# Performance work log

Measured on AMD Instinct MI355X. Metric: run time of the kernel, lower is better.

The kernel has to match this reference:

```python
import jax, jax.numpy as jnp
import numpy as np

H, HD, CHUNK = 16, 64, 128


def _rotary(x):
    # x: (B,H,N,d); rotary_embedding_torch default: interleaved pairs, theta=10000
    N, d = x.shape[-2], x.shape[-1]
    inv_freq = 1.0 / (10000.0 ** (jnp.arange(0, d, 2, dtype=jnp.float32) / d))
    ang = jnp.arange(N, dtype=jnp.float32)[:, None] * inv_freq[None, :]  # (N, d/2)
    ang = jnp.repeat(ang, 2, axis=-1)  # (N, d), each freq repeated twice
    cos, sin = jnp.cos(ang), jnp.sin(ang)
    x1, x2 = x[..., 0::2], x[..., 1::2]
    xr = jnp.stack([-x2, x1], axis=-1).reshape(x.shape)  # rotate_half (interleaved)
    return x * cos + xr * sin


def _split_heads(t, B, N):
    return t.reshape(B, N, H, HD).transpose(0, 2, 1, 3)  # (B,H,N,Hd)


def _chunked(Q, KK, VK):
    # chunk-parallel linear-attention recurrence: per-token outer products,
    # intra-chunk cumsum, carried state across chunks, Frobenius normalization.
    B, h, N, d = Q.shape
    nc = N // CHUNK

    def to_chunks(t):
        return t.reshape(B, h, nc, CHUNK, d).transpose(2, 0, 1, 3, 4)  # (nc,B,h,c,d)

    S0 = jnp.eye(d, dtype=Q.dtype) * jnp.sqrt(jnp.float32(d))
    S0 = jnp.broadcast_to(S0, (B, h, d, d))

    def step(SK_state, inp):
        q, kk, vk = inp  # (B,h,c,d)
        ok = jnp.einsum('bhni,bhnj->bhnij', kk, vk)            # outer products
        SK = jnp.cumsum(ok, axis=2) + SK_state[:, :, None]      # prefix-sum + carry
        norm = jnp.sqrt(jnp.sum(SK * SK, axis=(-2, -1), keepdims=True)) + 1e-8
        SKn = SK / norm                                         # Frobenius-normalized
        y = jnp.einsum('bhni,bhnji->bhnj', q, SKn)              # q @ SK^T per token
        return SK[:, :, -1], y

    _, ys = jax.lax.scan(step, S0, (to_chunks(Q), to_chunks(KK), to_chunks(VK)))
    return ys.transpose(1, 2, 0, 3, 4).reshape(B, h, N, d)


def setup_inputs():
    key = jax.random.key(0)
    ks = jax.random.split(key, 5)
    B, N, D = 2, 2048, 1024
    X = jax.random.normal(ks[0], (B, N, D), jnp.float32)
    w_qkv = jax.random.normal(ks[1], (D, 3 * H * HD), jnp.float32) * 0.02
    w_kvkv = jax.random.normal(ks[2], (D, 4 * H * HD), jnp.float32) * 0.02
    w_out = jax.random.normal(ks[3], (H * HD, D), jnp.float32) * 0.02
    b_out = jnp.zeros((D,), jnp.float32)
    return {"X": X, "w_qkv": w_qkv, "w_kvkv": w_kvkv, "w_out": w_out, "b_out": b_out}


def reference(X, w_qkv, w_kvkv, w_out, b_out):
    B, N, D = X.shape
    q, k, v = jnp.split(X @ w_qkv, 3, axis=-1)
    Q = _split_heads(q, B, N)
    K = _split_heads(k, B, N)
    V = _split_heads(v, B, N)
    kk, vk, _kv, _vv = jnp.split(X @ w_kvkv, 4, axis=-1)
    KK = _split_heads(kk, B, N)
    VK = _split_heads(vk, B, N)
    # NOTE: the SV branch (KV, VV) in the original is returned by the chunked fn
    # but never used by forward's output, so it is dead code for the fwd result.
    Qn = _chunked(Q, KK, VK)
    Qr = _rotary(Qn)
    Kr = _rotary(K)
    scale = 1.0 / jnp.sqrt(jnp.float32(HD))
    scores = jnp.einsum('bhqd,bhkd->bhqk', Qr, Kr) * scale
    mask = jnp.tril(jnp.ones((N, N), dtype=bool))
    scores = jnp.where(mask, scores, -jnp.inf)
    attn = jax.nn.softmax(scores, axis=-1)
    out = jnp.einsum('bhqk,bhkd->bhqd', attn, V)
    out = out.transpose(0, 2, 1, 3).reshape(B, N, H * HD)
    return out @ w_out + b_out
```

## Files before the change

kernel.cpp:

```cpp
#include <hip/hip_runtime.h>

typedef unsigned int u32;
typedef unsigned short u16;
typedef __attribute__((ext_vector_type(8))) __bf16 bf16x8;
typedef __attribute__((ext_vector_type(4))) float f32x4;

constexpr int NH = 16;
constexpr int HDM = 64;
constexpr int NSQ = 2048;
constexpr int KD = 1024;
constexpr int BHT = 32;
constexpr float ROT_C = 13.287712379549449f / 32.0f;

__device__ __forceinline__ u16 f2bf(float f) {
  u32 u = __float_as_uint(f);
  u += 0x7fffu + ((u >> 16) & 1u);
  return (u16)(u >> 16);
}
__device__ __forceinline__ float bf2f(u16 h) {
  return __uint_as_float(((u32)h) << 16);
}

__device__ __forceinline__ void fast_sincos(float th, float* s, float* c) {
  __sincosf(th, s, c);
}

__device__ __forceinline__ void gl_lds16(const u16* g, u16* l) {
  __builtin_amdgcn_global_load_lds(
      (const __attribute__((address_space(1))) u32*)g,
      (__attribute__((address_space(3))) u32*)l, 16, 0, 0);
}

__device__ __forceinline__ bf16x8 ldf(const u16* b, int row, int cb, int rs) {
  return *(const bf16x8*)((const char*)b + row * rs + ((cb * 16) ^ ((row & 7) << 4)));
}

__global__ void k_f32_to_bf16(const float* __restrict__ src, u16* __restrict__ dst, int n4) {
  int i = blockIdx.x * 256 + threadIdx.x;
  if (i < n4) {
    float4 v = ((const float4*)src)[i];
    ushort4 o;
    o.x = f2bf(v.x); o.y = f2bf(v.y); o.z = f2bf(v.z); o.w = f2bf(v.w);
    ((ushort4*)dst)[i] = o;
  }
}

__global__ void k_transpose_bf16(const float* __restrict__ src, int srcld,
                                 u16* __restrict__ dst, int dstld) {
  __shared__ float tile[64][65];
  int ct = blockIdx.x * 64, kt = blockIdx.y * 64;
  int lc = threadIdx.x & 63, rg = threadIdx.x >> 6;
#pragma unroll
  for (int i = 0; i < 16; ++i) {
    int kl = rg * 16 + i;
    tile[kl][lc] = src[(size_t)(kt + kl) * srcld + ct + lc];
  }
  __syncthreads();
#pragma unroll
  for (int i = 0; i < 16; ++i) {
    int cl = rg * 16 + i;
    dst[(size_t)(ct + cl) * dstld + kt + lc] = f2bf(tile[lc][cl]);
  }
}

template <int MODE>
__device__ __forceinline__ void gemm_stage(const u16* __restrict__ A, const u16* __restrict__ Bt,
                                           u16* Albuf, u16* Blbuf, int mt, int nt, int kt,
                                           int w, int lane) {
#pragma unroll
  for (int i = 0; i < 2; ++i) {
    int ob = (w * 2 + i) * 1024 + lane * 16;
    int row = ob >> 6;
    int ke = (ob & 63) >> 1;
    const u16* ga;
    if (MODE == 0) {
      ga = A + (size_t)(mt * 128 + row) * KD + kt * 32 + ke;
    } else {
      int grow = mt * 128 + row;
      int k = kt * 32 + ke;
      ga = A + ((size_t)((grow >> 11) * NH + (k >> 6)) * NSQ + (grow & 2047)) * HDM + (k & 63);
    }
    gl_lds16(ga, Albuf + (w * 2 + i) * 512);
    const u16* gb = Bt + (size_t)(nt * 128 + row) * KD + kt * 32 + ke;
    gl_lds16(gb, Blbuf + (w * 2 + i) * 512);
  }
}

__device__ __forceinline__ void gemm_compute(const u16* Albuf, const u16* Blbuf,
                                             f32x4 acc[4][4], int wr, int wc, int g, int q) {
  bf16x8 af[4], bfr[4];
#pragma unroll
  for (int m = 0; m < 4; ++m)
    af[m] = *(const bf16x8*)(Albuf + (wr * 64 + m * 16 + q) * 32 + g * 8);
#pragma unroll
  for (int n = 0; n < 4; ++n)
    bfr[n] = *(const bf16x8*)(Blbuf + (wc * 64 + n * 16 + q) * 32 + g * 8);
#pragma unroll
  for (int m = 0; m < 4; ++m)
#pragma unroll
    for (int n = 0; n < 4; ++n)
      acc[m][n] = __builtin_amdgcn_mfma_f32_16x16x32_bf16(af[m], bfr[n], acc[m][n], 0, 0, 0);
}

template <int MODE>
__global__ __launch_bounds__(256) void k_gemm(const u16* __restrict__ A, const u16* __restrict__ Bt,
                                              u16* __restrict__ o0, u16* __restrict__ o1,
                                              u16* __restrict__ o2, u16* __restrict__ o3,
                                              u16* __restrict__ o4,
                                              const float* __restrict__ bias,
                                              float* __restrict__ Cout) {
  __shared__ __align__(16) u16 Al[2][4096];
  __shared__ __align__(16) u16 Bl[2][4096];
  int nt = blockIdx.x, mt = blockIdx.y;
  int tid = threadIdx.x, w = tid >> 6, lane = tid & 63;
  int g = lane >> 4, q = lane & 15, wr = w >> 1, wc = w & 1;
  f32x4 acc[4][4];
#pragma unroll
  for (int m = 0; m < 4; ++m)
#pragma unroll
    for (int n = 0; n < 4; ++n) acc[m][n] = (f32x4){0.f, 0.f, 0.f, 0.f};

  gemm_stage<MODE>(A, Bt, Al[0], Bl[0], mt, nt, 0, w, lane);
  __syncthreads();
  int cur = 0;
  for (int kt = 1; kt < 32; ++kt) {
    gemm_stage<MODE>(A, Bt, Al[cur ^ 1], Bl[cur ^ 1], mt, nt, kt, w, lane);
    gemm_compute(Al[cur], Bl[cur], acc, wr, wc, g, q);
    __syncthreads();
    cur ^= 1;
  }
  gemm_compute(Al[cur], Bl[cur], acc, wr, wc, g, q);

  if (MODE == 0) {
#pragma unroll
    for (int nf = 0; nf < 4; ++nf) {
      int c = nt * 128 + wc * 64 + nf * 16 + q;
      if (c >= 1024 && c < 2048) {
        int rem = c - 1024;
        int hh = rem >> 6, dd = rem & 63;
        float invf = exp2f(-(float)(dd >> 1) * ROT_C);
        float sgn = (dd & 1) ? 1.0f : -1.0f;
        size_t hoff = (size_t)hh * NSQ * HDM + dd;
#pragma unroll
        for (int mf = 0; mf < 4; ++mf)
#pragma unroll
          for (int r = 0; r < 4; ++r) {
            int row = mt * 128 + wr * 64 + mf * 16 + g * 4 + r;
            int b = row >> 11, nn = row & 2047;
            float mine = acc[mf][nf][r];
            float part = __shfl_xor(mine, 1);
            float s, cc;
            fast_sincos((float)nn * invf, &s, &cc);
            o1[(size_t)b * NH * NSQ * HDM + hoff + (size_t)nn * HDM] = f2bf(mine * cc + sgn * part * s);
          }
      } else if (c >= 2048 && c < 3072) {
        int rem = c - 2048;
        int hh = rem >> 6, dd = rem & 63;
#pragma unroll
        for (int mf = 0; mf < 4; ++mf)
#pragma unroll
          for (int r = 0; r < 4; ++r) {
            int row = mt * 128 + wr * 64 + mf * 16 + g * 4 + r;
            int b = row >> 11, nn = row & 2047;
            o2[((size_t)(b * NH + hh) * HDM + dd) * NSQ + nn] = f2bf(acc[mf][nf][r]);
          }
      } else {
        u16* dst; int rem;
        if (c < 1024)      { dst = o0; rem = c; }
        else if (c < 4096) { dst = o3; rem = c - 3072; }
        else               { dst = o4; rem = c - 4096; }
        size_t hoff = (size_t)(rem >> 6) * NSQ * HDM + (rem & 63);
#pragma unroll
        for (int mf = 0; mf < 4; ++mf)
#pragma unroll
          for (int r = 0; r < 4; ++r) {
            int row = mt * 128 + wr * 64 + mf * 16 + g * 4 + r;
            int b = row >> 11, nn = row & 2047;
            dst[(size_t)b * NH * NSQ * HDM + hoff + (size_t)nn * HDM] = f2bf(acc[mf][nf][r]);
          }
      }
    }
  } else {
#pragma unroll
    for (int nf = 0; nf < 4; ++nf) {
      int c = nt * 128 + wc * 64 + nf * 16 + q;
      float bv = bias[c];
#pragma unroll
      for (int mf = 0; mf < 4; ++mf)
#pragma unroll
        for (int r = 0; r < 4; ++r) {
          int row = mt * 128 + wr * 64 + mf * 16 + g * 4 + r;
          Cout[(size_t)row * 1024 + c] = acc[mf][nf][r] + bv;
        }
    }
  }
}

__global__ __launch_bounds__(256) void k_chunk_outer(const u16* __restrict__ Kk,
                                                     const u16* __restrict__ Vk,
                                                     float* __restrict__ Mc) {
  int bhc = blockIdx.x;
  __shared__ float kk[128][64];
  __shared__ float vv[128][64];
  int tid = threadIdx.x;
  size_t base = ((size_t)(bhc >> 4) * NSQ + (size_t)(bhc & 15) * 128) * HDM;
  for (int i = tid; i < 2048; i += 256) {
    int r = i >> 4, c4 = (i & 15) * 4;
    ushort4 a = ((const ushort4*)(Kk + base))[i];
    kk[r][c4] = bf2f(a.x); kk[r][c4 + 1] = bf2f(a.y); kk[r][c4 + 2] = bf2f(a.z); kk[r][c4 + 3] = bf2f(a.w);
    ushort4 b = ((const ushort4*)(Vk + base))[i];
    vv[r][c4] = bf2f(b.x); vv[r][c4 + 1] = bf2f(b.y); vv[r][c4 + 2] = bf2f(b.z); vv[r][c4 + 3] = bf2f(b.w);
  }
  __syncthreads();
  int i0 = (tid >> 4) * 4, j0 = (tid & 15) * 4;
  float a2[4][4];
#pragma unroll
  for (int di = 0; di < 4; ++di)
#pragma unroll
    for (int dj = 0; dj < 4; ++dj) a2[di][dj] = 0.f;
  for (int m = 0; m < 128; ++m) {
    float ka[4], vb[4];
#pragma unroll
    for (int d = 0; d < 4; ++d) { ka[d] = kk[m][i0 + d]; vb[d] = vv[m][j0 + d]; }
#pragma unroll
    for (int di = 0; di < 4; ++di)
#pragma unroll
      for (int dj = 0; dj < 4; ++dj) a2[di][dj] += ka[di] * vb[dj];
  }
  float* out = Mc + (size_t)bhc * 4096;
#pragma unroll
  for (int di = 0; di < 4; ++di) {
    float4 v = make_float4(a2[di][0], a2[di][1], a2[di][2], a2[di][3]);
    *(float4*)(out + (i0 + di) * 64 + j0) = v;
  }
}

__global__ __launch_bounds__(256) void k_chunk_prefix2(const float* __restrict__ Mc,
                                                       float* __restrict__ Sst) {
  int bh = blockIdx.x, rg = blockIdx.y;
  int tid = threadIdx.x;
  int r8 = tid >> 5, cp = tid & 31;
  int i = rg * 8 + r8, j0 = cp * 2;
  float s0 = (i == j0) ? 8.0f : 0.0f;
  float s1 = (i == j0 + 1) ? 8.0f : 0.0f;
  size_t rowoff = (size_t)i * 64 + j0;
  for (int c = 0; c < 16; ++c) {
    size_t o = ((size_t)bh * 16 + c) * 4096 + rowoff;
    *(float2*)(Sst + o) = make_float2(s0, s1);
    float2 mv = *(const float2*)(Mc + o);
    s0 += mv.x; s1 += mv.y;
  }
}

__global__ __launch_bounds__(256) void k_chunk_norm(const u16* __restrict__ Kk,
                                                    const u16* __restrict__ Vk,
                                                    const float* __restrict__ Sst,
                                                    float* __restrict__ Invn) {
  __shared__ __align__(16) u16 KkL[128 * 64];
  __shared__ __align__(16) u16 VkL[128 * 64];
  __shared__ __align__(16) u16 SL[64 * 64];
  __shared__ float prebuf[128][2];
  __shared__ float bilbuf[128][2];
  __shared__ float sc[128];
  __shared__ float red[4];
  int bhc = blockIdx.x;
  int tid = threadIdx.x, w = tid >> 6, lane = tid & 63;
  int g = lane >> 4, q = lane & 15;
  size_t base = (size_t)bhc * 8192;

  for (int ic = tid; ic < 1024; ic += 256) {
    int row = ic >> 3, cb = ic & 7;
    int off = row * 128 + ((cb * 16) ^ ((row & 7) << 4));
    *(uint4*)((char*)KkL + off) = ((const uint4*)(Kk + base))[ic];
    *(uint4*)((char*)VkL + off) = ((const uint4*)(Vk + base))[ic];
  }
  float ss = 0.f;
  const float4* Sg = (const float4*)(Sst + (size_t)bhc * 4096);
  for (int i = tid; i < 1024; i += 256) {
    float4 v = Sg[i];
    ss += v.x * v.x + v.y * v.y + v.z * v.z + v.w * v.w;
    int row = i >> 4, c8 = (i & 15) * 8;
    u32 lo = (u32)f2bf(v.x) | ((u32)f2bf(v.y) << 16);
    u32 hi = (u32)f2bf(v.z) | ((u32)f2bf(v.w) << 16);
    *(uint2*)((char*)SL + row * 128 + (c8 ^ ((row & 7) << 4))) = make_uint2(lo, hi);
  }
#pragma unroll
  for (int d = 1; d < 64; d <<= 1) ss += __shfl_xor(ss, d);
  if (lane == 0) red[w] = ss;
  __syncthreads();

  int wr = w >> 1, wc = w & 1;
  bf16x8 ka[4][2], va[4][2];
#pragma unroll
  for (int mf = 0; mf < 4; ++mf)
#pragma unroll
    for (int ks = 0; ks < 2; ++ks) {
      ka[mf][ks] = ldf(KkL, wr * 64 + mf * 16 + q, ks * 4 + g, 128);
      va[mf][ks] = ldf(VkL, wr * 64 + mf * 16 + q, ks * 4 + g, 128);
    }

  float pracc[4][4];
#pragma unroll
  for (int mf = 0; mf < 4; ++mf)
#pragma unroll
    for (int r = 0; r < 4; ++r) pracc[mf][r] = 0.f;
  for (int pf = 0; pf < 4; ++pf) {
    bf16x8 kb0 = ldf(KkL, wc * 64 + pf * 16 + q, g, 128);
    bf16x8 kb1 = ldf(KkL, wc * 64 + pf * 16 + q, 4 + g, 128);
    bf16x8 vb0 = ldf(VkL, wc * 64 + pf * 16 + q, g, 128);
    bf16x8 vb1 = ldf(VkL, wc * 64 + pf * 16 + q, 4 + g, 128);
#pragma unroll
    for (int mf = 0; mf < 4; ++mf) {
      f32x4 a1 = (f32x4){0.f, 0.f, 0.f, 0.f}, b1 = (f32x4){0.f, 0.f, 0.f, 0.f};
      a1 = __builtin_amdgcn_mfma_f32_16x16x32_bf16(ka[mf][0], kb0, a1, 0, 0, 0);
      a1 = __builtin_amdgcn_mfma_f32_16x16x32_bf16(ka[mf][1], kb1, a1, 0, 0, 0);
      b1 = __builtin_amdgcn_mfma_f32_16x16x32_bf16(va[mf][0], vb0, b1, 0, 0, 0);
      b1 = __builtin_amdgcn_mfma_f32_16x16x32_bf16(va[mf][1], vb1, b1, 0, 0, 0);
#pragma unroll
      for (int r = 0; r < 4; ++r) {
        int m = wr * 64 + mf * 16 + g * 4 + r;
        int p = wc * 64 + pf * 16 + q;
        float gv = a1[r] * b1[r];
        float coef = (p < m) ? 1.f : ((p == m) ? 0.5f : 0.f);
        pracc[mf][r] += coef * gv;
      }
    }
  }
#pragma unroll
  for (int mf = 0; mf < 4; ++mf)
#pragma unroll
    for (int r = 0; r < 4; ++r) {
      float v = pracc[mf][r];
      v += __shfl_xor(v, 1); v += __shfl_xor(v, 2); v += __shfl_xor(v, 4); v += __shfl_xor(v, 8);
      pracc[mf][r] = v;
    }
  if (q == 0) {
#pragma unroll
    for (int mf = 0; mf < 4; ++mf)
#pragma unroll
      for (int r = 0; r < 4; ++r) prebuf[wr * 64 + mf * 16 + g * 4 + r][wc] = pracc[mf][r];
  }

  float bacc[4][4];
#pragma unroll
  for (int mf = 0; mf < 4; ++mf)
#pragma unroll
    for (int r = 0; r < 4; ++r) bacc[mf][r] = 0.f;
  for (int jf = 0; jf < 2; ++jf) {
    bf16x8 sb0 = ldf(SL, wc * 32 + jf * 16 + q, g, 128);
    bf16x8 sb1 = ldf(SL, wc * 32 + jf * 16 + q, 4 + g, 128);
#pragma unroll
    for (int mf = 0; mf < 4; ++mf) {
      f32x4 u = (f32x4){0.f, 0.f, 0.f, 0.f};
      u = __builtin_amdgcn_mfma_f32_16x16x32_bf16(va[mf][0], sb0, u, 0, 0, 0);
      u = __builtin_amdgcn_mfma_f32_16x16x32_bf16(va[mf][1], sb1, u, 0, 0, 0);
#pragma unroll
      for (int r = 0; r < 4; ++r) {
        int m = wr * 64 + mf * 16 + g * 4 + r;
        int j = wc * 32 + jf * 16 + q;
        float kkv = bf2f(*(const u16*)((const char*)KkL + m * 128 + ((j * 2) ^ ((m & 7) << 4))));
        bacc[mf][r] += u[r] * kkv;
      }
    }
  }
#pragma unroll
  for (int mf = 0; mf < 4; ++mf)
#pragma unroll
    for (int r = 0; r < 4; ++r) {
      float v = bacc[mf][r];
      v += __shfl_xor(v, 1); v += __shfl_xor(v, 2); v += __shfl_xor(v, 4); v += __shfl_xor(v, 8);
      bacc[mf][r] = v;
    }
  if (q == 0) {
#pragma unroll
    for (int mf = 0; mf < 4; ++mf)
#pragma unroll
      for (int r = 0; r < 4; ++r) bilbuf[wr * 64 + mf * 16 + g * 4 + r][wc] = bacc[mf][r];
  }
  __syncthreads();

  if (tid < 128)
    sc[tid] = 2.f * (prebuf[tid][0] + prebuf[tid][1] + bilbuf[tid][0] + bilbuf[tid][1]);
  __syncthreads();
  for (int off = 1; off < 128; off <<= 1) {
    float add = 0.f;
    if (tid < 128 && tid >= off) add = sc[tid - off];
    __syncthreads();
    if (tid < 128) sc[tid] += add;
    __syncthreads();
  }
  if (tid < 128) {
    float n0 = red[0] + red[1] + red[2] + red[3];
    float cum = n0 + sc[tid];
    Invn[(size_t)bhc * 128 + tid] = 1.f / (sqrtf(cum) + 1e-8f);
  }
}

__global__ __launch_bounds__(256) void k_chunk_yv2(const u16* __restrict__ Qb,
                                                   const u16* __restrict__ Kk,
                                                   const u16* __restrict__ Vk,
                                                   const float* __restrict__ Sst,
                                                   const float* __restrict__ Invn,
                                                   u16* __restrict__ Qro) {
  __shared__ __align__(16) u16 QL[128 * 64];
  __shared__ __align__(16) u16 WL[128 * 64];
  __shared__ __align__(16) u16 SL[64 * 64];
  __shared__ __align__(16) u16 PL[128 * 128];
  __shared__ float inv[128];
  int bhc = blockIdx.x;
  int tid = threadIdx.x, w = tid >> 6, lane = tid & 63;
  int g = lane >> 4, q = lane & 15;
  size_t base = (size_t)bhc * 8192;

  for (int ic = tid; ic < 1024; ic += 256) {
    int row = ic >> 3, cb = ic & 7;
    int off = row * 128 + ((cb * 16) ^ ((row & 7) << 4));
    *(uint4*)((char*)QL + off) = ((const uint4*)(Qb + base))[ic];
    *(uint4*)((char*)WL + off) = ((const uint4*)(Vk + base))[ic];
  }
  const float4* Sg = (const float4*)(Sst + (size_t)bhc * 4096);
  for (int i = tid; i < 1024; i += 256) {
    float4 v = Sg[i];
    int row = i >> 4, c8 = (i & 15) * 8;
    u32 lo = (u32)f2bf(v.x) | ((u32)f2bf(v.y) << 16);
    u32 hi = (u32)f2bf(v.z) | ((u32)f2bf(v.w) << 16);
    *(uint2*)((char*)SL + row * 128 + (c8 ^ ((row & 7) << 4))) = make_uint2(lo, hi);
  }
  if (tid < 128) inv[tid] = Invn[(size_t)bhc * 128 + tid];
  __syncthreads();

  int wr = w >> 1, wc = w & 1;
  f32x4 pacc[4][4];
#pragma unroll
  for (int mf = 0; mf < 4; ++mf)
#pragma unroll
    for (int nf = 0; nf < 4; ++nf) pacc[mf][nf] = (f32x4){0.f, 0.f, 0.f, 0.f};
#pragma unroll
  for (int ks = 0; ks < 2; ++ks) {
    bf16x8 av[4], bq[4];
#pragma unroll
    for (int mf = 0; mf < 4; ++mf) av[mf] = ldf(WL, wr * 64 + mf * 16 + q, ks * 4 + g, 128);
#pragma unroll
    for (int nf = 0; nf < 4; ++nf) bq[nf] = ldf(QL, wc * 64 + nf * 16 + q, ks * 4 + g, 128);
#pragma unroll
    for (int mf = 0; mf < 4; ++mf)
#pragma unroll
      for (int nf = 0; nf < 4; ++nf)
        pacc[mf][nf] = __builtin_amdgcn_mfma_f32_16x16x32_bf16(av[mf], bq[nf], pacc[mf][nf], 0, 0, 0);
  }
#pragma unroll
  for (int mf = 0; mf < 4; ++mf)
#pragma unroll
    for (int nf = 0; nf < 4; ++nf) {
      int m0 = wr * 64 + mf * 16 + g * 4;
      int n = wc * 64 + nf * 16 + q;
      float v0 = (m0 + 0 <= n) ? pacc[mf][nf][0] : 0.f;
      float v1 = (m0 + 1 <= n) ? pacc[mf][nf][1] : 0.f;
      float v2 = (m0 + 2 <= n) ? pacc[mf][nf][2] : 0.f;
      float v3 = (m0 + 3 <= n) ? pacc[mf][nf][3] : 0.f;
      u32 lo = (u32)f2bf(v0) | ((u32)f2bf(v1) << 16);
      u32 hi = (u32)f2bf(v2) | ((u32)f2bf(v3) << 16);
      *(uint2*)((char*)PL + n * 256 + ((m0 * 2) ^ ((n & 7) << 4))) = make_uint2(lo, hi);
    }
  __syncthreads();
  for (int i = tid; i < 2048; i += 256) {
    int r = i >> 4, c4 = (i & 15) * 4;
    ushort4 kv = ((const ushort4*)(Kk + base))[i];
    *(u16*)((char*)WL + (c4 + 0) * 256 + ((r * 2) ^ (((c4 + 0) & 7) << 4))) = kv.x;
    *(u16*)((char*)WL + (c4 + 1) * 256 + ((r * 2) ^ (((c4 + 1) & 7) << 4))) = kv.y;
    *(u16*)((char*)WL + (c4 + 2) * 256 + ((r * 2) ^ (((c4 + 2) & 7) << 4))) = kv.z;
    *(u16*)((char*)WL + (c4 + 3) * 256 + ((r * 2) ^ (((c4 + 3) & 7) << 4))) = kv.w;
  }
  __syncthreads();

  f32x4 yacc[4][2];
#pragma unroll
  for (int nf = 0; nf < 4; ++nf)
#pragma unroll
    for (int jf = 0; jf < 2; ++jf) yacc[nf][jf] = (f32x4){0.f, 0.f, 0.f, 0.f};
#pragma unroll
  for (int ks = 0; ks < 2; ++ks) {
    bf16x8 aq[4], bs[2];
#pragma unroll
    for (int nf = 0; nf < 4; ++nf) aq[nf] = ldf(QL, wr * 64 + nf * 16 + q, ks * 4 + g, 128);
#pragma unroll
    for (int jf = 0; jf < 2; ++jf) bs[jf] = ldf(SL, wc * 32 + jf * 16 + q, ks * 4 + g, 128);
#pragma unroll
    for (int nf = 0; nf < 4; ++nf)
#pragma unroll
      for (int jf = 0; jf < 2; ++jf)
        yacc[nf][jf] = __builtin_amdgcn_mfma_f32_16x16x32_bf16(aq[nf], bs[jf], yacc[nf][jf], 0, 0, 0);
  }
#pragma unroll
  for (int ks = 0; ks < 4; ++ks) {
    bf16x8 ap[4], bk[2];
#pragma unroll
    for (int nf = 0; nf < 4; ++nf) ap[nf] = ldf(PL, wr * 64 + nf * 16 + q, ks * 4 + g, 256);
#pragma unroll
    for (int jf = 0; jf < 2; ++jf) bk[jf] = ldf(WL, wc * 32 + jf * 16 + q, ks * 4 + g, 256);
#pragma unroll
    for (int nf = 0; nf < 4; ++nf)
#pragma unroll
      for (int jf = 0; jf < 2; ++jf)
        yacc[nf][jf] = __builtin_amdgcn_mfma_f32_16x16x32_bf16(ap[nf], bk[jf], yacc[nf][jf], 0, 0, 0);
  }
#pragma unroll
  for (int nf = 0; nf < 4; ++nf)
#pragma unroll
    for (int jf = 0; jf < 2; ++jf) {
      int j = wc * 32 + jf * 16 + q;
      float invf = exp2f(-(float)(j >> 1) * ROT_C);
      float sgn = (j & 1) ? 1.0f : -1.0f;
#pragma unroll
      for (int r = 0; r < 4; ++r) {
        int n = wr * 64 + nf * 16 + g * 4 + r;
        float val = yacc[nf][jf][r] * inv[n];
        float part = __shfl_xor(val, 1);
        int ng = (bhc & 15) * 128 + n;
        float s, cc;
        fast_sincos((float)ng * invf, &s, &cc);
        Qro[base + (size_t)n * 64 + j] = f2bf((val * cc + sgn * part * s) * 0.125f);
      }
    }
}

__global__ __launch_bounds__(512) void k_attn2(const u16* __restrict__ Qr, const u16* __restrict__ Kr,
                                               const u16* __restrict__ Vt, u16* __restrict__ Ob) {
  __shared__ __align__(16) u16 QL[128 * 64];
  __shared__ __align__(16) u16 KL[2][64 * 64];
  __shared__ __align__(16) u16 VL[2][64 * 64];
  __shared__ __align__(16) u16 PLa[8][16 * 64];
  int bh = blockIdx.x, pair = blockIdx.y;
  int tid = threadIdx.x, w = tid >> 6, lane = tid & 63;
  int g = lane >> 4, q16 = lane & 15;
  const u16* Qg_base = Qr + (size_t)bh * NSQ * HDM;
  const u16* Kg_base = Kr + (size_t)bh * NSQ * HDM;
  const u16* VTg_base = Vt + (size_t)bh * HDM * NSQ;
  u16* Og_base = Ob + (size_t)bh * NSQ * HDM;
  u16* Pw = PLa[w];
  int srow = tid >> 3, scb = tid & 7;

  for (int phase = 0; phase < 2; ++phase) {
    int t = phase ? (15 - pair) : pair;
    int qbase = t * 128;
    int nkt = 2 * t + 2;
    int lastkt_w = (qbase + w * 16 + 15) >> 6;
    int qg_ = qbase + w * 16 + q16;

    {
      const u16* Qg = Qg_base + qbase * 64;
#pragma unroll
      for (int it = 0; it < 2; ++it) {
        int c = it * 512 + tid;
        int row = c >> 3, cb = c & 7;
        gl_lds16(Qg + row * 64 + ((cb ^ (row & 7)) << 3), QL + c * 8);
      }
    }
    gl_lds16(Kg_base + srow * 64 + ((scb ^ (srow & 7)) << 3), KL[0] + tid * 8);
    gl_lds16(VTg_base + (size_t)srow * NSQ + ((scb ^ (srow & 7)) << 3), VL[0] + tid * 8);
    __syncthreads();

    bf16x8 qf[2];
    qf[0] = ldf(QL, w * 16 + q16, g, 128);
    qf[1] = ldf(QL, w * 16 + q16, 4 + g, 128);

    f32x4 o[4];
#pragma unroll
    for (int df = 0; df < 4; ++df) o[df] = (f32x4){0.f, 0.f, 0.f, 0.f};
    float m_run = -3.0e38f, l_run = 0.f;

    int cur = 0;
    for (int kt = 0; kt < nkt; ++kt) {
      if (kt + 1 < nkt) {
        gl_lds16(Kg_base + (kt + 1) * 4096 + srow * 64 + ((scb ^ (srow & 7)) << 3),
                 KL[cur ^ 1] + tid * 8);
        gl_lds16(VTg_base + (size_t)srow * NSQ + (kt + 1) * 64 + ((scb ^ (srow & 7)) << 3),
                 VL[cur ^ 1] + tid * 8);
      }
      if (kt <= lastkt_w) {
        const u16* Kbuf = KL[cur];
        const u16* Vbuf = VL[cur];
        f32x4 st[4];
#pragma unroll
        for (int kf = 0; kf < 4; ++kf) {
          f32x4 s = (f32x4){0.f, 0.f, 0.f, 0.f};
          s = __builtin_amdgcn_mfma_f32_16x16x32_bf16(ldf(Kbuf, kf * 16 + q16, g, 128), qf[0], s, 0, 0, 0);
          s = __builtin_amdgcn_mfma_f32_16x16x32_bf16(ldf(Kbuf, kf * 16 + q16, 4 + g, 128), qf[1], s, 0, 0, 0);
          st[kf] = s;
        }
        float smax = -1e30f;
        bool needmask = (kt * 64 + 63 > qbase + w * 16);
        if (needmask) {
#pragma unroll
          for (int kf = 0; kf < 4; ++kf)
#pragma unroll
            for (int r = 0; r < 4; ++r) {
              int keyg = kt * 64 + kf * 16 + g * 4 + r;
              float sv = st[kf][r];
              sv = (keyg <= qg_) ? sv : -1e30f;
              st[kf][r] = sv;
              smax = fmaxf(smax, sv);
            }
        } else {
#pragma unroll
          for (int kf = 0; kf < 4; ++kf)
#pragma unroll
            for (int r = 0; r < 4; ++r) smax = fmaxf(smax, st[kf][r]);
        }
        smax = fmaxf(smax, __shfl_xor(smax, 16));
        smax = fmaxf(smax, __shfl_xor(smax, 32));
        float mnew = fmaxf(m_run, smax);
        float corr = __expf(m_run - mnew);
        float ls = 0.f;
#pragma unroll
        for (int kf = 0; kf < 4; ++kf)
#pragma unroll
          for (int r = 0; r < 4; ++r) {
            float p = __expf(st[kf][r] - mnew);
            st[kf][r] = p;
            ls += p;
          }
        ls += __shfl_xor(ls, 16);
        ls += __shfl_xor(ls, 32);
        m_run = mnew;
        l_run = l_run * corr + ls;
#pragma unroll
        for (int df = 0; df < 4; ++df) {
          o[df][0] *= corr; o[df][1] *= corr; o[df][2] *= corr; o[df][3] *= corr;
        }
#pragma unroll
        for (int kf = 0; kf < 4; ++kf) {
          u32 lo = (u32)f2bf(st[kf][0]) | ((u32)f2bf(st[kf][1]) << 16);
          u32 hi = (u32)f2bf(st[kf][2]) | ((u32)f2bf(st[kf][3]) << 16);
          int ba = q16 * 128 + ((kf * 32 + g * 8) ^ ((q16 & 7) << 4));
          *(u32*)((char*)Pw + ba) = lo;
          *(u32*)((char*)Pw + ba + 4) = hi;
        }
#pragma unroll
        for (int kc = 0; kc < 2; ++kc) {
          bf16x8 pf = ldf(Pw, q16, kc * 4 + g, 128);
#pragma unroll
          for (int df = 0; df < 4; ++df) {
            bf16x8 vf = ldf(Vbuf, df * 16 + q16, kc * 4 + g, 128);
            o[df] = __builtin_amdgcn_mfma_f32_16x16x32_bf16(vf, pf, o[df], 0, 0, 0);
          }
        }
      }
      __syncthreads();
      cur ^= 1;
    }
    float invl = 1.0f / l_run;
    u16* Og = Og_base + (size_t)(qbase + w * 16 + q16) * HDM;
#pragma unroll
    for (int df = 0; df < 4; ++df)
#pragma unroll
      for (int r = 0; r < 4; ++r) Og[df * 16 + g * 4 + r] = f2bf(o[df][r] * invl);
  }
}

extern "C" void kernel_launch(void* const* d_in, const int* in_sizes, int n_in,
                              void* d_out, int out_size, void* d_ws, size_t ws_size,
                              hipStream_t stream) {
  const float* X = (const float*)d_in[0];
  const float* w_qkv = (const float*)d_in[1];
  const float* w_kvkv = (const float*)d_in[2];
  const float* w_out = (const float*)d_in[3];
  const float* b_out = (const float*)d_in[4];
  float* out = (float*)d_out;
  char* ws = (char*)d_ws;

  u16* Xb  = (u16*)(ws + 0);
  u16* WbT = (u16*)(ws + 8388608);
  u16* WoT = (u16*)(ws + 18874368);
  u16* Qb  = (u16*)(ws + 20971520);
  float* Sst = (float*)(ws + 29360128);
  u16* Vtb = (u16*)(ws + 37748736);
  u16* Kkb = (u16*)(ws + 46137344);
  u16* Vkb = (u16*)(ws + 54525952);
  u16* Kr  = (u16*)(ws + 62914560);
  u16* Qr  = (u16*)(ws + 71303168);
  float* Mc   = (float*)(ws + 8388608);
  float* Invn = (float*)(ws + 16777216);
  u16* Ob = (u16*)(ws + 0);
  (void)in_sizes; (void)n_in; (void)out_size; (void)ws_size;

  k_f32_to_bf16<<<dim3(4096), dim3(256), 0, stream>>>(X, Xb, 1048576);
  k_transpose_bf16<<<dim3(48, 16), dim3(256), 0, stream>>>(w_qkv, 3072, WbT, 1024);
  k_transpose_bf16<<<dim3(32, 16), dim3(256), 0, stream>>>(w_kvkv, 4096, WbT + (size_t)3072 * 1024, 1024);
  k_transpose_bf16<<<dim3(16, 16), dim3(256), 0, stream>>>(w_out, 1024, WoT, 1024);
  k_gemm<0><<<dim3(40, 32), dim3(256), 0, stream>>>(Xb, WbT, Qb, Kr, Vtb, Kkb, Vkb, nullptr, nullptr);
  k_chunk_outer<<<dim3(512), dim3(256), 0, stream>>>(Kkb, Vkb, Mc);
  k_chunk_prefix2<<<dim3(32, 8), dim3(256), 0, stream>>>(Mc, Sst);
  k_chunk_norm<<<dim3(512), dim3(256), 0, stream>>>(Kkb, Vkb, Sst, Invn);
  k_chunk_yv2<<<dim3(512), dim3(256), 0, stream>>>(Qb, Kkb, Vkb, Sst, Invn, Qr);
  k_attn2<<<dim3(32, 8), dim3(512), 0, stream>>>(Qr, Kr, Vtb, Ob);
  k_gemm<1><<<dim3(8, 32), dim3(256), 0, stream>>>(Ob, WoT, nullptr, nullptr, nullptr, nullptr, nullptr, b_out, out);
}
```

Measured before the change: 208.0 us.

## Rewrite input projection GEMM with 256x256 tiles, swizzled LDS and deeper prefetch

Replaces the fused QKV/KV projection GEMM with a dedicated kernel that uses 256x256 output tiles, 512 threads, a K-step of 64, and an XOR-swizzled LDS layout to avoid bank conflicts. It prefetches two stages ahead with explicit vmcnt waits and raw barriers, raises wave priority around the MFMA blocks, and remaps block IDs so neighbouring blocks share operand tiles in cache. The aim is more data reuse per LDS byte and better overlap of loads with matrix math. In exchange it uses 128KB of LDS and many accumulator registers, which lowers occupancy, and only 320 blocks are launched. The output GEMM is split out unchanged.

```diff
diff --git a/kernel.cpp b/kernel.cpp
--- a/kernel.cpp
+++ b/kernel.cpp
@@ -63,31 +63,166 @@
   }
 }
 
-template <int MODE>
-__device__ __forceinline__ void gemm_stage(const u16* __restrict__ A, const u16* __restrict__ Bt,
-                                           u16* Albuf, u16* Blbuf, int mt, int nt, int kt,
-                                           int w, int lane) {
+__device__ __forceinline__ void stage256(const u16* __restrict__ gA, const u16* __restrict__ gB,
+                                         u16* AL, u16* BL, int mt, int nt, int kt, int tid) {
+#pragma unroll
+  for (int l = 0; l < 4; ++l) {
+    int off = l * 8192 + tid * 16;
+    int row = off >> 7;
+    int cb = (off >> 4) & 7;
+    int col = (cb ^ (row & 7)) << 3;
+    gl_lds16(gA + (size_t)(mt * 256 + row) * KD + kt * 64 + col, AL + (off >> 1));
+  }
+#pragma unroll
+  for (int l = 0; l < 4; ++l) {
+    int off = l * 8192 + tid * 16;
+    int row = off >> 7;
+    int cb = (off >> 4) & 7;
+    int col = (cb ^ (row & 7)) << 3;
+    gl_lds16(gB + (size_t)(nt * 256 + row) * KD + kt * 64 + col, BL + (off >> 1));
+  }
+}
+
+__device__ __forceinline__ void compute256(const u16* AL, const u16* BL,
+                                           f32x4 (&acc)[8][4], int wr, int wc, int g, int q) {
+#pragma unroll
+  for (int ks = 0; ks < 2; ++ks) {
+    bf16x8 bfr[4];
+#pragma unroll
+    for (int nf = 0; nf < 4; ++nf)
+      bfr[nf] = ldf(BL, wc * 64 + nf * 16 + q, ks * 4 + g, 128);
+#pragma unroll
+    for (int mh = 0; mh < 2; ++mh) {
+      bf16x8 af[4];
+#pragma unroll
+      for (int mf = 0; mf < 4; ++mf)
+        af[mf] = ldf(AL, wr * 128 + (mh * 4 + mf) * 16 + q, ks * 4 + g, 128);
+      __builtin_amdgcn_s_setprio(1);
+#pragma unroll
+      for (int mf = 0; mf < 4; ++mf)
+#pragma unroll
+        for (int nf = 0; nf < 4; ++nf)
+          acc[mh * 4 + mf][nf] =
+              __builtin_amdgcn_mfma_f32_16x16x32_bf16(af[mf], bfr[nf], acc[mh * 4 + mf][nf], 0, 0, 0);
+      __builtin_amdgcn_s_setprio(0);
+    }
+  }
+}
+
+__global__ __launch_bounds__(512) void k_gemm0_256(const u16* __restrict__ A,
+                                                   const u16* __restrict__ Bt,
+                                                   u16* __restrict__ o0, u16* __restrict__ o1,
+                                                   u16* __restrict__ o2, u16* __restrict__ o3,
+                                                   u16* __restrict__ o4) {
+  __shared__ __align__(16) u16 AL[2][16384];
+  __shared__ __align__(16) u16 BL[2][16384];
+  int bid = blockIdx.x;
+  int swz = (bid & 7) * 40 + (bid >> 3);
+  int nt = swz % 20, mt = swz / 20;
+  int tid = threadIdx.x, w = tid >> 6, lane = tid & 63;
+  int g = lane >> 4, q = lane & 15;
+  int wr = w >> 2, wc = w & 3;
+
+  f32x4 acc[8][4];
+#pragma unroll
+  for (int m = 0; m < 8; ++m)
+#pragma unroll
+    for (int n = 0; n < 4; ++n) acc[m][n] = (f32x4){0.f, 0.f, 0.f, 0.f};
+
+  stage256(A, Bt, AL[0], BL[0], mt, nt, 0, tid);
+  stage256(A, Bt, AL[1], BL[1], mt, nt, 1, tid);
+  asm volatile("s_waitcnt vmcnt(8)" ::: "memory");
+  __builtin_amdgcn_s_barrier();
+  __builtin_amdgcn_sched_barrier(0);
+
+#define GBODY(KT, PBUF)                                                     \
+  {                                                                         \
+    compute256(AL[PBUF], BL[PBUF], acc, wr, wc, g, q);                      \
+    __builtin_amdgcn_s_barrier();                                           \
+    if ((KT) + 2 < 16) {                                                    \
+      stage256(A, Bt, AL[PBUF], BL[PBUF], mt, nt, (KT) + 2, tid);           \
+      asm volatile("s_waitcnt vmcnt(8)" ::: "memory");                      \
+    } else if ((KT) == 14) {                                                \
+      asm volatile("s_waitcnt vmcnt(0)" ::: "memory");                      \
+    }                                                                       \
+    __builtin_amdgcn_s_barrier();                                           \
+    __builtin_amdgcn_sched_barrier(0);                                      \
+  }
+
+  for (int it = 0; it < 8; ++it) {
+    GBODY(2 * it, 0);
+    GBODY(2 * it + 1, 1);
+  }
+#undef GBODY
+
+#pragma unroll
+  for (int nf = 0; nf < 4; ++nf) {
+    int c = nt * 256 + wc * 64 + nf * 16 + q;
+    int t = c >> 10;
+    if (t == 1) {
+      int rem = c & 1023;
+      int hh = rem >> 6, dd = rem & 63;
+      float invf = exp2f(-(float)(dd >> 1) * ROT_C);
+      float sgn = (dd & 1) ? 1.0f : -1.0f;
+      size_t hoff = (size_t)hh * NSQ * HDM + dd;
+#pragma unroll
+      for (int mf = 0; mf < 8; ++mf)
+#pragma unroll
+        for (int r = 0; r < 4; ++r) {
+          int row = mt * 256 + wr * 128 + mf * 16 + g * 4 + r;
+          int b = row >> 11, nn = row & 2047;
+          float mine = acc[mf][nf][r];
+          float part = __shfl_xor(mine, 1);
+          float s, cc;
+          fast_sincos((float)nn * invf, &s, &cc);
+          o1[(size_t)b * NH * NSQ * HDM + hoff + (size_t)nn * HDM] = f2bf(mine * cc + sgn * part * s);
+        }
+    } else if (t == 2) {
+      int rem = c & 1023;
+      int hh = rem >> 6, dd = rem & 63;
+#pragma unroll
+      for (int mf = 0; mf < 8; ++mf)
+#pragma unroll
+        for (int r = 0; r < 4; ++r) {
+          int row = mt * 256 + wr * 128 + mf * 16 + g * 4 + r;
+          int b = row >> 11, nn = row & 2047;
+          o2[((size_t)(b * NH + hh) * HDM + dd) * NSQ + nn] = f2bf(acc[mf][nf][r]);
+        }
+    } else {
+      u16* dst = (t == 0) ? o0 : ((t == 3) ? o3 : o4);
+      int rem = c & 1023;
+      size_t hoff = (size_t)(rem >> 6) * NSQ * HDM + (rem & 63);
+#pragma unroll
+      for (int mf = 0; mf < 8; ++mf)
+#pragma unroll
+        for (int r = 0; r < 4; ++r) {
+          int row = mt * 256 + wr * 128 + mf * 16 + g * 4 + r;
+          int b = row >> 11, nn = row & 2047;
+          dst[(size_t)b * NH * NSQ * HDM + hoff + (size_t)nn * HDM] = f2bf(acc[mf][nf][r]);
+        }
+    }
+  }
+}
+
+__device__ __forceinline__ void gemm_stage1(const u16* __restrict__ A, const u16* __restrict__ Bt,
+                                            u16* Albuf, u16* Blbuf, int mt, int nt, int kt,
+                                            int w, int lane) {
 #pragma unroll
   for (int i = 0; i < 2; ++i) {
     int ob = (w * 2 + i) * 1024 + lane * 16;
     int row = ob >> 6;
     int ke = (ob & 63) >> 1;
-    const u16* ga;
-    if (MODE == 0) {
-      ga = A + (size_t)(mt * 128 + row) * KD + kt * 32 + ke;
-    } else {
-      int grow = mt * 128 + row;
-      int k = kt * 32 + ke;
-      ga = A + ((size_t)((grow >> 11) * NH + (k >> 6)) * NSQ + (grow & 2047)) * HDM + (k & 63);
-    }
+    int grow = mt * 128 + row;
+    int k = kt * 32 + ke;
+    const u16* ga = A + ((size_t)((grow >> 11) * NH + (k >> 6)) * NSQ + (grow & 2047)) * HDM + (k & 63);
     gl_lds16(ga, Albuf + (w * 2 + i) * 512);
     const u16* gb = Bt + (size_t)(nt * 128 + row) * KD + kt * 32 + ke;
     gl_lds16(gb, Blbuf + (w * 2 + i) * 512);
   }
 }
 
-__device__ __forceinline__ void gemm_compute(const u16* Albuf, const u16* Blbuf,
-                                             f32x4 acc[4][4], int wr, int wc, int g, int q) {
+__device__ __forceinline__ void gemm_compute1(const u16* Albuf, const u16* Blbuf,
+                                              f32x4 acc[4][4], int wr, int wc, int g, int q) {
   bf16x8 af[4], bfr[4];
 #pragma unroll
   for (int m = 0; m < 4; ++m)
@@ -102,13 +237,9 @@
       acc[m][n] = __builtin_amdgcn_mfma_f32_16x16x32_bf16(af[m], bfr[n], acc[m][n], 0, 0, 0);
 }
 
-template <int MODE>
-__global__ __launch_bounds__(256) void k_gemm(const u16* __restrict__ A, const u16* __restrict__ Bt,
-                                              u16* __restrict__ o0, u16* __restrict__ o1,
-                                              u16* __restrict__ o2, u16* __restrict__ o3,
-                                              u16* __restrict__ o4,
-                                              const float* __restrict__ bias,
-                                              float* __restrict__ Cout) {
+__global__ __launch_bounds__(256) void k_gemm_out(const u16* __restrict__ A, const u16* __restrict__ Bt,
+                                                  const float* __restrict__ bias,
+                                                  float* __restrict__ Cout) {
   __shared__ __align__(16) u16 Al[2][4096];
   __shared__ __align__(16) u16 Bl[2][4096];
   int nt = blockIdx.x, mt = blockIdx.y;
@@ -120,79 +251,28 @@
 #pragma unroll
     for (int n = 0; n < 4; ++n) acc[m][n] = (f32x4){0.f, 0.f, 0.f, 0.f};
 
-  gemm_stage<MODE>(A, Bt, Al[0], Bl[0], mt, nt, 0, w, lane);
+  gemm_stage1(A, Bt, Al[0], Bl[0], mt, nt, 0, w, lane);
   __syncthreads();
   int cur = 0;
   for (int kt = 1; kt < 32; ++kt) {
-    gemm_stage<MODE>(A, Bt, Al[cur ^ 1], Bl[cur ^ 1], mt, nt, kt, w, lane);
-    gemm_compute(Al[cur], Bl[cur], acc, wr, wc, g, q);
+    gemm_stage1(A, Bt, Al[cur ^ 1], Bl[cur ^ 1], mt, nt, kt, w, lane);
+    gemm_compute1(Al[cur], Bl[cur], acc, wr, wc, g, q);
     __syncthreads();
     cur ^= 1;
   }
-  gemm_compute(Al[cur], Bl[cur], acc, wr, wc, g, q);
-
-  if (MODE == 0) {
-#pragma unroll
-    for (int nf = 0; nf < 4; ++nf) {
-      int c = nt * 128 + wc * 64 + nf * 16 + q;
-      if (c >= 1024 && c < 2048) {
-        int rem = c - 1024;
-        int hh = rem >> 6, dd = rem & 63;
-        float invf = exp2f(-(float)(dd >> 1) * ROT_C);
-        float sgn = (dd & 1) ? 1.0f : -1.0f;
-        size_t hoff = (size_t)hh * NSQ * HDM + dd;
-#pragma unroll
-        for (int mf = 0; mf < 4; ++mf)
-#pragma unroll
-          for (int r = 0; r < 4; ++r) {
-            int row = mt * 128 + wr * 64 + mf * 16 + g * 4 + r;
-            int b = row >> 11, nn = row & 2047;
-            float mine = acc[mf][nf][r];
-            float part = __shfl_xor(mine, 1);
-            float s, cc;
-            fast_sincos((float)nn * invf, &s, &cc);
-            o1[(size_t)b * NH * NSQ * HDM + hoff + (size_t)nn * HDM] = f2bf(mine * cc + sgn * part * s);
-          }
-      } else if (c >= 2048 && c < 3072) {
-        int rem = c - 2048;
-        int hh = rem >> 6, dd = rem & 63;
-#pragma unroll
-        for (int mf = 0; mf < 4; ++mf)
-#pragma unroll
-          for (int r = 0; r < 4; ++r) {
-            int row = mt * 128 + wr * 64 + mf * 16 + g * 4 + r;
-            int b = row >> 11, nn = row & 2047;
-            o2[((size_t)(b * NH + hh) * HDM + dd) * NSQ + nn] = f2bf(acc[mf][nf][r]);
-          }
-      } else {
-        u16* dst; int rem;
-        if (c < 1024)      { dst = o0; rem = c; }
-        else if (c < 4096) { dst = o3; rem = c - 3072; }
-        else               { dst = o4; rem = c - 4096; }
-        size_t hoff = (size_t)(rem >> 6) * NSQ * HDM + (rem & 63);
-#pragma unroll
-        for (int mf = 0; mf < 4; ++mf)
-#pragma unroll
-          for (int r = 0; r < 4; ++r) {
-            int row = mt * 128 + wr * 64 + mf * 16 + g * 4 + r;
-            int b = row >> 11, nn = row & 2047;
-            dst[(size_t)b * NH * NSQ * HDM + hoff + (size_t)nn * HDM] = f2bf(acc[mf][nf][r]);
-          }
+  gemm_compute1(Al[cur], Bl[cur], acc, wr, wc, g, q);
+
+#pragma unroll
+  for (int nf = 0; nf < 4; ++nf) {
+    int c = nt * 128 + wc * 64 + nf * 16 + q;
+    float bv = bias[c];
+#pragma unroll
+    for (int mf = 0; mf < 4; ++mf)
+#pragma unroll
+      for (int r = 0; r < 4; ++r) {
+        int row = mt * 128 + wr * 64 + mf * 16 + g * 4 + r;
+        Cout[(size_t)row * 1024 + c] = acc[mf][nf][r] + bv;
       }
-    }
-  } else {
-#pragma unroll
-    for (int nf = 0; nf < 4; ++nf) {
-      int c = nt * 128 + wc * 64 + nf * 16 + q;
-      float bv = bias[c];
-#pragma unroll
-      for (int mf = 0; mf < 4; ++mf)
-#pragma unroll
-        for (int r = 0; r < 4; ++r) {
-          int row = mt * 128 + wr * 64 + mf * 16 + g * 4 + r;
-          Cout[(size_t)row * 1024 + c] = acc[mf][nf][r] + bv;
-        }
-    }
   }
 }
 
@@ -688,11 +768,11 @@
   k_transpose_bf16<<<dim3(48, 16), dim3(256), 0, stream>>>(w_qkv, 3072, WbT, 1024);
   k_transpose_bf16<<<dim3(32, 16), dim3(256), 0, stream>>>(w_kvkv, 4096, WbT + (size_t)3072 * 1024, 1024);
   k_transpose_bf16<<<dim3(16, 16), dim3(256), 0, stream>>>(w_out, 1024, WoT, 1024);
-  k_gemm<0><<<dim3(40, 32), dim3(256), 0, stream>>>(Xb, WbT, Qb, Kr, Vtb, Kkb, Vkb, nullptr, nullptr);
+  k_gemm0_256<<<dim3(320), dim3(512), 0, stream>>>(Xb, WbT, Qb, Kr, Vtb, Kkb, Vkb);
   k_chunk_outer<<<dim3(512), dim3(256), 0, stream>>>(Kkb, Vkb, Mc);
   k_chunk_prefix2<<<dim3(32, 8), dim3(256), 0, stream>>>(Mc, Sst);
   k_chunk_norm<<<dim3(512), dim3(256), 0, stream>>>(Kkb, Vkb, Sst, Invn);
   k_chunk_yv2<<<dim3(512), dim3(256), 0, stream>>>(Qb, Kkb, Vkb, Sst, Invn, Qr);
   k_attn2<<<dim3(32, 8), dim3(512), 0, stream>>>(Qr, Kr, Vtb, Ob);
-  k_gemm<1><<<dim3(8, 32), dim3(256), 0, stream>>>(Ob, WoT, nullptr, nullptr, nullptr, nullptr, nullptr, b_out, out);
-}
+  k_gemm_out<<<dim3(8, 32), dim3(256), 0, stream>>>(Ob, WoT, b_out, out);
+}
```

New measurement: 196.8 us. 5.4% less time.
